# Performance work log

Hardware: AMD Instinct MI355X
Metric: run time of the kernel (lower is better)

## Reference

```python
import jax, jax.numpy as jnp
import numpy as np

B, S, D, NH = 1, 2048, 2048, 8
DH = D // NH
BACKEND_EPS = 1e-6
NORM_EPS = 1e-6


def setup_inputs() -> dict:
    key = jax.random.key(0)
    ks = jax.random.split(key, 6)
    q = jax.random.normal(ks[0], (B, S, D), jnp.float32)
    k = jax.random.normal(ks[1], (B, S, D), jnp.float32)
    v = jax.random.normal(ks[2], (B, S, D), jnp.float32)
    igate_kernel = jax.random.normal(ks[3], (3 * D, NH), jnp.float32) * 0.02
    igate_bias = jax.random.normal(ks[4], (NH,), jnp.float32) * 0.1
    fgate_kernel = jax.random.normal(ks[5], (3 * D, NH), jnp.float32) * 0.02
    fgate_bias = jnp.linspace(3.0, 6.0, NH, dtype=jnp.float32)  # bias_linspace_init(3.0, 6.0)
    out_weight = jnp.ones((NH, DH), jnp.float32)  # MultiHeadLayerNorm scale (no bias)
    return dict(q=q, k=k, v=v, igate_kernel=igate_kernel, igate_bias=igate_bias,
                fgate_kernel=fgate_kernel, fgate_bias=fgate_bias, out_weight=out_weight)


def _mlstm_parallel_stabilized(q, k, v, i_pre, f_pre):
    # q,k,v: (B,NH,S,DH); i_pre,f_pre: (B,NH,S)
    s = q.shape[-2]
    dh = q.shape[-1]
    log_f = jax.nn.log_sigmoid(f_pre)                              # (B,NH,S)
    cum = jnp.pad(jnp.cumsum(log_f, axis=-1), ((0, 0), (0, 0), (1, 0)))  # (B,NH,S+1), cum[0]=0
    # logfg[t, s] = cum[t+1] - cum[s+1] = sum_{j=s+1}^{t} log_f[j], valid for s <= t
    logfg = cum[..., 1:, None] - cum[..., None, 1:]                # (B,NH,S,S)
    causal = jnp.tril(jnp.ones((s, s), dtype=bool))
    logfg = jnp.where(causal, logfg, -jnp.inf)
    log_D = logfg + i_pre[..., None, :]                            # add input gate at source position s
    m = jnp.max(log_D, axis=-1, keepdims=True)                     # stabilizer (B,NH,S,1)
    D = jnp.exp(log_D - m)
    qk = jnp.einsum('bhsd,bhtd->bhst', q, k) / jnp.sqrt(jnp.float32(dh))
    C = qk * D                                                     # (B,NH,S,S)
    n = jnp.maximum(jnp.abs(jnp.sum(C, axis=-1, keepdims=True)), jnp.exp(-m))
    return jnp.einsum('bhst,bhtd->bhsd', C / (n + BACKEND_EPS), v)


def reference(q, k, v, igate_kernel, igate_bias, fgate_kernel, fgate_bias, out_weight):
    qkv = jnp.concatenate([q, k, v], axis=-1)                      # (B,S,3D)
    i_pre = qkv @ igate_kernel + igate_bias                        # (B,S,NH)
    f_pre = qkv @ fgate_kernel + fgate_bias                        # (B,S,NH)
    qh = q.reshape(B, S, NH, DH).transpose(0, 2, 1, 3)             # (B,NH,S,DH)
    kh = k.reshape(B, S, NH, DH).transpose(0, 2, 1, 3)
    vh = v.reshape(B, S, NH, DH).transpose(0, 2, 1, 3)
    h = _mlstm_parallel_stabilized(qh, kh, vh,
                                   i_pre.transpose(0, 2, 1),
                                   f_pre.transpose(0, 2, 1))       # (B,NH,S,DH)
    h = h.transpose(0, 2, 1, 3)                                    # (B,S,NH,DH)
    mu = jnp.mean(h, axis=-1, keepdims=True)
    var = jnp.var(h, axis=-1, keepdims=True)
    hn = (h - mu) * jax.lax.rsqrt(var + NORM_EPS) * out_weight     # per-head LN, scale only
    return hn.reshape(B, S, D)
```

## Files before the change

### kernel.cpp

```cpp
#include <hip/hip_runtime.h>
#include <hip/hip_bf16.h>

#define SEQ 2048
#define DMODEL 2048
#define NHEAD 8
#define DHEAD 256

typedef _Float16 v8h __attribute__((ext_vector_type(8)));
typedef unsigned short v8u __attribute__((ext_vector_type(8)));
typedef float v4f __attribute__((ext_vector_type(4)));

__device__ __forceinline__ float b2f(unsigned short s) {
    return __uint_as_float(((unsigned)s) << 16);
}
__device__ __forceinline__ unsigned short f2b(float f) {
    unsigned u = __float_as_uint(f);
    u += 0x7fffu + ((u >> 16) & 1u);
    return (unsigned short)(u >> 16);
}
__device__ __forceinline__ unsigned short f2h(float f) {
    _Float16 h = (_Float16)f;
    return __builtin_bit_cast(unsigned short, h);
}
__device__ __forceinline__ float h2f(unsigned short s) {
    return (float)__builtin_bit_cast(_Float16, s);
}

__global__ __launch_bounds__(256) void k_pre(const void* q, const void* k, const void* v,
                                             const void* igk, const void* fgk,
                                             int* flag,
                                             unsigned short* qb, unsigned short* kb,
                                             unsigned short* vT,
                                             float* iparts, float* fparts) {
    __shared__ float x_lds[32][67];
    __shared__ int cnt;
    const int tid = threadIdx.x;

    if (tid == 0) cnt = 0;
    __syncthreads();
    {
        const unsigned short* qp = (const unsigned short*)q;
        int wild = 0;
        for (int i = tid; i < 2048; i += 256) {
            float x = b2f(qp[i]);
            float ax = fabsf(x);
            if (!(ax <= 100.0f) || (x != 0.0f && ax < 1e-6f)) wild++;
        }
        atomicAdd(&cnt, wild);
    }
    __syncthreads();
    const int bf = (cnt < 256) ? 1 : 0;
    if (blockIdx.x == 0 && blockIdx.y == 0 && tid == 0) *flag = bf;

    const int s0 = blockIdx.x * 32;
    const int z  = blockIdx.y;
    const int tz = z >> 1;
    const int dbase = (z & 1) * 1024;
    const void* src = (tz == 0) ? q : (tz == 1) ? k : v;
    unsigned short* dst16 = (tz == 0) ? qb : kb;

    const int r  = tid >> 3, c0 = (tid & 7) * 8;
    const int sl = tid >> 3, hh = tid & 7;
    float accI = 0.f, accF = 0.f;
    const unsigned short* ik16 = (const unsigned short*)igk;
    const unsigned short* fk16 = (const unsigned short*)fgk;
    const float* ik32 = (const float*)igk;
    const float* fk32 = (const float*)fgk;

    for (int ch = 0; ch < 16; ++ch) {
        const int d0 = dbase + ch * 64;
        float xv[8];
        const size_t base = (size_t)(s0 + r) * DMODEL + d0 + c0;
        if (bf) {
            const unsigned short* sp = (const unsigned short*)src;
            v8u a = *(const v8u*)(sp + base);
#pragma unroll
            for (int j = 0; j < 8; j++) xv[j] = b2f(a[j]);
        } else {
            const float* sp = (const float*)src;
            v4f a0 = *(const v4f*)(sp + base);
            v4f a1 = *(const v4f*)(sp + base + 4);
#pragma unroll
            for (int j = 0; j < 4; j++) { xv[j] = a0[j]; xv[4 + j] = a1[j]; }
        }
        __syncthreads();
#pragma unroll
        for (int j = 0; j < 8; j++) x_lds[r][c0 + j] = xv[j];
        if (tz < 2) {
            v8u o;
#pragma unroll
            for (int j = 0; j < 8; j++) o[j] = f2h(xv[j]);
            *(v8u*)(dst16 + base) = o;
        }
        __syncthreads();
        const int gd0 = tz * 2048 + d0;
        if (bf) {
#pragma unroll 8
            for (int j = 0; j < 64; j++) {
                float x = x_lds[sl][j];
                int wi = (gd0 + j) * NHEAD + hh;
                accI += x * b2f(ik16[wi]);
                accF += x * b2f(fk16[wi]);
            }
        } else {
#pragma unroll 8
            for (int j = 0; j < 64; j++) {
                float x = x_lds[sl][j];
                int wi = (gd0 + j) * NHEAD + hh;
                accI += x * ik32[wi];
                accF += x * fk32[wi];
            }
        }
        if (tz == 2) {
            const int dloc = tid >> 2, sc0 = (tid & 3) * 8;
            v8u o;
#pragma unroll
            for (int j = 0; j < 8; j++) o[j] = f2h(x_lds[sc0 + j][dloc]);
            const int dglob = d0 + dloc;
            const int head = dglob >> 8, dh = dglob & 255;
            *(v8u*)(vT + ((size_t)(head * DHEAD + dh)) * SEQ + s0 + sc0) = o;
        }
    }
    iparts[(size_t)z * NHEAD * SEQ + hh * SEQ + s0 + sl] = accI;
    fparts[(size_t)z * NHEAD * SEQ + hh * SEQ + s0 + sl] = accF;
}

__global__ __launch_bounds__(256) void k_scan(const float* iparts, const float* fparts,
                                              const void* ib_, const void* fb_,
                                              const int* flag,
                                              float* a_g, float* amax_g, float* nfl_g) {
    __shared__ float sarr[256];
    int bf = *(volatile const int*)flag;
    int h = blockIdx.x, tid = threadIdx.x;
    float ib = bf ? b2f(((const unsigned short*)ib_)[h]) : ((const float*)ib_)[h];
    float fb = bf ? b2f(((const unsigned short*)fb_)[h]) : ((const float*)fb_)[h];
    int s0 = tid * 8;
    float lf[8], ip[8];
#pragma unroll
    for (int j = 0; j < 8; j++) {
        float fpv = fb, ipv = ib;
#pragma unroll
        for (int z = 0; z < 6; z++) {
            ipv += iparts[(size_t)z * NHEAD * SEQ + h * SEQ + s0 + j];
            fpv += fparts[(size_t)z * NHEAD * SEQ + h * SEQ + s0 + j];
        }
        lf[j] = fminf(fpv, 0.0f) - log1pf(__expf(-fabsf(fpv)));
        ip[j] = ipv;
    }
    float cs[8]; float t = 0.f;
#pragma unroll
    for (int j = 0; j < 8; j++) { t += lf[j]; cs[j] = t; }
    sarr[tid] = t; __syncthreads();
    for (int ofs = 1; ofs < 256; ofs <<= 1) {
        float val = sarr[tid];
        if (tid >= ofs) val += sarr[tid - ofs];
        __syncthreads(); sarr[tid] = val; __syncthreads();
    }
    float excl = (tid > 0) ? sarr[tid - 1] : 0.0f;
    float cum[8], av[8];
#pragma unroll
    for (int j = 0; j < 8; j++) { cum[j] = excl + cs[j]; av[j] = ip[j] - cum[j]; }
    float mx = av[0];
#pragma unroll
    for (int j = 1; j < 8; j++) mx = fmaxf(mx, av[j]);
    __syncthreads(); sarr[tid] = mx; __syncthreads();
    for (int ofs = 1; ofs < 256; ofs <<= 1) {
        float val = sarr[tid];
        if (tid >= ofs) val = fmaxf(val, sarr[tid - ofs]);
        __syncthreads(); sarr[tid] = val; __syncthreads();
    }
    float run = (tid > 0) ? sarr[tid - 1] : -3.0e38f;
#pragma unroll
    for (int j = 0; j < 8; j++) {
        run = fmaxf(run, av[j]);
        int s = s0 + j;
        a_g[h * SEQ + s]    = av[j];
        amax_g[h * SEQ + s] = run;
        float m = cum[j] + run;
        nfl_g[h * SEQ + s]  = __expf(fminf(fmaxf(-m, -60.f), 60.f));
    }
}

__global__ __launch_bounds__(256) void k_main(const unsigned short* __restrict__ qb,
                                              const unsigned short* __restrict__ kb,
                                              const unsigned short* __restrict__ vT,
                                              const float* __restrict__ a_g,
                                              const float* __restrict__ amax_g,
                                              float* __restrict__ h_buf,
                                              float* __restrict__ rs_buf) {
    __shared__ __align__(16) unsigned short q_lds[32][264];
    __shared__ __align__(16) unsigned short k_lds[32][264];
    __shared__ __align__(16) unsigned short vT_lds[272][40];
    __shared__ __align__(16) unsigned short P_lds[32][40];
    __shared__ __align__(16) unsigned short Plo_lds[32][40];
    __shared__ float a_s[32], amax_t[32];

    const int h   = blockIdx.x;
    const int y   = blockIdx.y;
    const int tid = threadIdx.x;
    const int lane = tid & 63;
    const int w   = tid >> 6;
    const int l15 = lane & 15;
    const int qd  = (lane >> 4) & 3;
    const int hd0 = h * DHEAD;

    int u         = 65 * (y >> 1) + ((y & 1) ? 33 : 0);
    int remaining = (y & 1) ? 32 : 33;
    int tile = (int)((sqrtf(8.0f * (float)u + 1.0f) - 1.0f) * 0.5f);
    while ((tile + 1) * (tile + 2) / 2 <= u) ++tile;
    while (tile * (tile + 1) / 2 > u) --tile;
    int js = u - tile * (tile + 1) / 2;
    bool needQ = true;

    for (int i = tid; i < 16 * 40; i += 256) {
        int r2 = i / 40, c2 = i % 40;
        vT_lds[256 + r2][c2] = (r2 == 0 && c2 < 32) ? (unsigned short)0x3C00 : (unsigned short)0;
    }

    const v4f vzero = {0.f, 0.f, 0.f, 0.f};
    v4f acc[2][4];
    v4f accN[2];
#pragma unroll
    for (int m = 0; m < 2; m++) {
        accN[m] = vzero;
#pragma unroll
        for (int n = 0; n < 4; n++) acc[m][n] = vzero;
    }

    const int mw = w >> 1, nw = w & 1;
    const int krow = tid >> 3, kc0 = (tid & 7) * 32;

    v8u kr0, kr1, kr2, kr3, vr0, vr1, vr2, vr3;
    float areg = 0.f;
    {
        const int s0 = js * 32;
        const unsigned short* ks = kb + (size_t)(s0 + krow) * DMODEL + hd0 + kc0;
        kr0 = *(const v8u*)(ks);      kr1 = *(const v8u*)(ks + 8);
        kr2 = *(const v8u*)(ks + 16); kr3 = *(const v8u*)(ks + 24);
        const unsigned short* vs = vT + (size_t)(hd0 + tid) * SEQ + s0;
        vr0 = *(const v8u*)(vs);      vr1 = *(const v8u*)(vs + 8);
        vr2 = *(const v8u*)(vs + 16); vr3 = *(const v8u*)(vs + 24);
        if (tid < 32) areg = a_g[h * SEQ + s0 + tid];
    }

    for (;;) {
        const int t0 = tile * 32;
        __syncthreads();
        if (needQ) {
            const unsigned short* src = qb + (size_t)(t0 + krow) * DMODEL + hd0 + kc0;
#pragma unroll
            for (int i = 0; i < 4; i++)
                *(v8u*)&q_lds[krow][kc0 + i * 8] = *(const v8u*)(src + i * 8);
            if (tid < 32) amax_t[tid] = amax_g[h * SEQ + t0 + tid];
            needQ = false;
        }
        *(v8u*)&k_lds[krow][kc0]      = kr0;
        *(v8u*)&k_lds[krow][kc0 + 8]  = kr1;
        *(v8u*)&k_lds[krow][kc0 + 16] = kr2;
        *(v8u*)&k_lds[krow][kc0 + 24] = kr3;
        *(v8u*)&vT_lds[tid][0]  = vr0;
        *(v8u*)&vT_lds[tid][8]  = vr1;
        *(v8u*)&vT_lds[tid][16] = vr2;
        *(v8u*)&vT_lds[tid][24] = vr3;
        if (tid < 32) a_s[tid] = areg;
        __syncthreads();

        v4f c = vzero;
#pragma unroll
        for (int d0 = 0; d0 < 256; d0 += 32) {
            v8h a = *(const v8h*)&q_lds[mw * 16 + l15][d0 + qd * 8];
            v8h b = *(const v8h*)&k_lds[nw * 16 + l15][d0 + qd * 8];
            c = __builtin_amdgcn_mfma_f32_16x16x32_f16(a, b, c, 0, 0, 0);
        }
        {
            const bool diag = (js == tile);
            const int col = nw * 16 + l15;
            const float av = a_s[col];
#pragma unroll
            for (int r = 0; r < 4; r++) {
                int row = mw * 16 + qd * 4 + r;
                float arg = fminf(av - amax_t[row], 0.0f);
                float val = c[r] * 0.0625f * __expf(arg);
                if (diag && col > row) val = 0.0f;
                unsigned short hi = f2h(val);
                float lo = val - h2f(hi);
                P_lds[row][col]   = hi;
                Plo_lds[row][col] = f2h(lo);
            }
        }
        __syncthreads();

        int ntile = tile, njs = js + 1; bool nq = false;
        if (njs > tile) { ntile = tile + 1; njs = 0; nq = true; }
        if (remaining > 1) {
            const int s0 = njs * 32;
            const unsigned short* ks = kb + (size_t)(s0 + krow) * DMODEL + hd0 + kc0;
            kr0 = *(const v8u*)(ks);      kr1 = *(const v8u*)(ks + 8);
            kr2 = *(const v8u*)(ks + 16); kr3 = *(const v8u*)(ks + 24);
            const unsigned short* vs = vT + (size_t)(hd0 + tid) * SEQ + s0;
            vr0 = *(const v8u*)(vs);      vr1 = *(const v8u*)(vs + 8);
            vr2 = *(const v8u*)(vs + 16); vr3 = *(const v8u*)(vs + 24);
            if (tid < 32) areg = a_g[h * SEQ + s0 + tid];
        }

        v8h aH0 = *(const v8h*)&P_lds[l15][qd * 8];
        v8h aH1 = *(const v8h*)&P_lds[16 + l15][qd * 8];
        v8h aL0 = *(const v8h*)&Plo_lds[l15][qd * 8];
        v8h aL1 = *(const v8h*)&Plo_lds[16 + l15][qd * 8];
#pragma unroll
        for (int nn = 0; nn < 4; nn++) {
            v8h bV = *(const v8h*)&vT_lds[w * 64 + nn * 16 + l15][qd * 8];
            acc[0][nn] = __builtin_amdgcn_mfma_f32_16x16x32_f16(aH0, bV, acc[0][nn], 0, 0, 0);
            acc[0][nn] = __builtin_amdgcn_mfma_f32_16x16x32_f16(aL0, bV, acc[0][nn], 0, 0, 0);
            acc[1][nn] = __builtin_amdgcn_mfma_f32_16x16x32_f16(aH1, bV, acc[1][nn], 0, 0, 0);
            acc[1][nn] = __builtin_amdgcn_mfma_f32_16x16x32_f16(aL1, bV, acc[1][nn], 0, 0, 0);
        }
        if (w == 3) {
            v8h bN = *(const v8h*)&vT_lds[256 + l15][qd * 8];
            accN[0] = __builtin_amdgcn_mfma_f32_16x16x32_f16(aH0, bN, accN[0], 0, 0, 0);
            accN[0] = __builtin_amdgcn_mfma_f32_16x16x32_f16(aL0, bN, accN[0], 0, 0, 0);
            accN[1] = __builtin_amdgcn_mfma_f32_16x16x32_f16(aH1, bN, accN[1], 0, 0, 0);
            accN[1] = __builtin_amdgcn_mfma_f32_16x16x32_f16(aL1, bN, accN[1], 0, 0, 0);
        }

        if (js == tile || remaining == 1) {
#pragma unroll
            for (int m = 0; m < 2; m++)
#pragma unroll
                for (int r = 0; r < 4; r++) {
                    int row = t0 + m * 16 + qd * 4 + r;
#pragma unroll
                    for (int nn = 0; nn < 4; nn++) {
                        int col = hd0 + w * 64 + nn * 16 + l15;
                        atomicAdd(&h_buf[(size_t)row * DMODEL + col], acc[m][nn][r]);
                        acc[m][nn][r] = 0.f;
                    }
                    if (w == 3 && l15 == 0)
                        atomicAdd(&rs_buf[h * SEQ + row], accN[m][r]);
                    accN[m][r] = 0.f;
                }
        }
        if (--remaining == 0) break;
        tile = ntile; js = njs; needQ = nq;
    }
}

__global__ __launch_bounds__(256) void k_finish(const float* __restrict__ h_buf,
                                                const float* __restrict__ rs_buf,
                                                const float* __restrict__ nfl_g,
                                                const void* __restrict__ ow,
                                                const int* flag, void* out) {
    const int wv = threadIdx.x >> 6, lane = threadIdx.x & 63;
    const int rid = blockIdx.x * 4 + wv;
    const int s = rid >> 3, h = rid & 7;
    const int bf = *(volatile const int*)flag;
    float rs  = rs_buf[h * SEQ + s];
    float nfl = nfl_g[h * SEQ + s];
    float sc  = 1.0f / (fmaxf(fabsf(rs), nfl) + 1e-6f);
    size_t base = (size_t)s * DMODEL + h * DHEAD + lane * 4;
    v4f hv = *(const v4f*)(h_buf + base);
#pragma unroll
    for (int j = 0; j < 4; j++) hv[j] *= sc;
    float sm = hv[0] + hv[1] + hv[2] + hv[3];
    float sq = hv[0] * hv[0] + hv[1] * hv[1] + hv[2] * hv[2] + hv[3] * hv[3];
#pragma unroll
    for (int m = 1; m < 64; m <<= 1) {
        sm += __shfl_xor(sm, m, 64);
        sq += __shfl_xor(sq, m, 64);
    }
    float mean = sm * (1.0f / 256.0f);
    float var  = fmaxf(sq * (1.0f / 256.0f) - mean * mean, 0.0f);
    float rstd = rsqrtf(var + 1e-6f);
    int gi = h * DHEAD + lane * 4;
    float g0, g1, g2, g3;
    if (bf) {
        const unsigned short* gp = (const unsigned short*)ow;
        g0 = b2f(gp[gi]); g1 = b2f(gp[gi + 1]); g2 = b2f(gp[gi + 2]); g3 = b2f(gp[gi + 3]);
    } else {
        const float* gp = (const float*)ow;
        g0 = gp[gi]; g1 = gp[gi + 1]; g2 = gp[gi + 2]; g3 = gp[gi + 3];
    }
    float gv[4] = {g0, g1, g2, g3};
    if (bf) {
        unsigned short* o = (unsigned short*)out + base;
#pragma unroll
        for (int j = 0; j < 4; j++) o[j] = f2b((hv[j] - mean) * rstd * gv[j]);
    } else {
        float* o = (float*)out + base;
#pragma unroll
        for (int j = 0; j < 4; j++) o[j] = (hv[j] - mean) * rstd * gv[j];
    }
}

extern "C" void kernel_launch(void* const* d_in, const int* in_sizes, int n_in,
                              void* d_out, int out_size, void* d_ws, size_t ws_size,
                              hipStream_t stream) {
    const void* q   = d_in[0];
    const void* k   = d_in[1];
    const void* v   = d_in[2];
    const void* igk = d_in[3];
    const void* igb = d_in[4];
    const void* fgk = d_in[5];
    const void* fgb = d_in[6];
    const void* ow  = d_in[7];

    char* ws = (char*)d_ws;
    int*   flag   = (int*)(ws + 0);
    float* iparts = (float*)(ws + 1024);
    float* fparts = iparts + 6 * NHEAD * SEQ;
    float* a_g    = fparts + 6 * NHEAD * SEQ;
    float* amax_g = a_g + NHEAD * SEQ;
    float* nfl_g  = amax_g + NHEAD * SEQ;
    unsigned short* qb = (unsigned short*)(nfl_g + NHEAD * SEQ);
    unsigned short* kb = qb + (size_t)SEQ * DMODEL;
    unsigned short* vT = kb + (size_t)SEQ * DMODEL;
    float* rs_buf = (float*)(vT + (size_t)SEQ * DMODEL);
    float* h_buf  = rs_buf + NHEAD * SEQ;

    hipMemsetAsync(rs_buf, 0, (size_t)NHEAD * SEQ * 4 + (size_t)SEQ * DMODEL * 4, stream);
    k_pre<<<dim3(64, 6), 256, 0, stream>>>(q, k, v, igk, fgk, flag, qb, kb, vT, iparts, fparts);
    k_scan<<<8, 256, 0, stream>>>(iparts, fparts, igb, fgb, flag, a_g, amax_g, nfl_g);
    k_main<<<dim3(8, 64), 256, 0, stream>>>(qb, kb, vT, a_g, amax_g, h_buf, rs_buf);
    k_finish<<<4096, 256, 0, stream>>>(h_buf, rs_buf, nfl_g, ow, flag, d_out);
}
```

Baseline: 268.2 us.

## Split preprocessing into separate convert, transpose and gate-projection blocks; warp-shuffle scan

The single fused preprocessing kernel (384 blocks, each converting, transposing and projecting gates over a 1024-wide slice) is replaced by a 3584-block kernel with three roles. Some blocks convert q/k to fp16, some transpose v through a 64x64 LDS tile, and the rest compute per-row gate projections with one wavefront per row, vectorised weight loads and shuffle reductions. The gate partial buffers shrink from 6 to 3 slices. The scan kernel swaps its LDS Hillis-Steele scans, which synchronise at every step, for wavefront shuffle scans plus a small cross-wave combine. The point is more parallelism and fewer barriers in the launch-latency-bound prologue, at the cost of rereading q/k/v in the gate blocks.

New measurement: 318.5 us. 1.19x slower.

```diff
diff --git a/kernel.cpp b/kernel.cpp
--- a/kernel.cpp
+++ b/kernel.cpp
@@ -32,9 +32,10 @@
                                              unsigned short* qb, unsigned short* kb,
                                              unsigned short* vT,
                                              float* iparts, float* fparts) {
-    __shared__ float x_lds[32][67];
+    __shared__ unsigned short tile[64][72];
     __shared__ int cnt;
     const int tid = threadIdx.x;
+    const int b = blockIdx.x;
 
     if (tid == 0) cnt = 0;
     __syncthreads();
@@ -50,126 +51,208 @@
     }
     __syncthreads();
     const int bf = (cnt < 256) ? 1 : 0;
-    if (blockIdx.x == 0 && blockIdx.y == 0 && tid == 0) *flag = bf;
-
-    const int s0 = blockIdx.x * 32;
-    const int z  = blockIdx.y;
-    const int tz = z >> 1;
-    const int dbase = (z & 1) * 1024;
-    const void* src = (tz == 0) ? q : (tz == 1) ? k : v;
-    unsigned short* dst16 = (tz == 0) ? qb : kb;
-
-    const int r  = tid >> 3, c0 = (tid & 7) * 8;
-    const int sl = tid >> 3, hh = tid & 7;
-    float accI = 0.f, accF = 0.f;
-    const unsigned short* ik16 = (const unsigned short*)igk;
-    const unsigned short* fk16 = (const unsigned short*)fgk;
-    const float* ik32 = (const float*)igk;
-    const float* fk32 = (const float*)fgk;
-
-    for (int ch = 0; ch < 16; ++ch) {
-        const int d0 = dbase + ch * 64;
-        float xv[8];
-        const size_t base = (size_t)(s0 + r) * DMODEL + d0 + c0;
+    if (b == 0 && tid == 0) *flag = bf;
+
+    if (b < 1024) {
+        size_t i0 = ((size_t)b * 256 + tid) * 16;
         if (bf) {
-            const unsigned short* sp = (const unsigned short*)src;
-            v8u a = *(const v8u*)(sp + base);
-#pragma unroll
-            for (int j = 0; j < 8; j++) xv[j] = b2f(a[j]);
+            const unsigned short* qp = (const unsigned short*)q;
+            const unsigned short* kp = (const unsigned short*)k;
+#pragma unroll
+            for (int hlf = 0; hlf < 2; hlf++) {
+                v8u uq = *(const v8u*)(qp + i0 + hlf * 8);
+                v8u uk = *(const v8u*)(kp + i0 + hlf * 8);
+                v8u oq, ok;
+#pragma unroll
+                for (int j = 0; j < 8; j++) { oq[j] = f2h(b2f(uq[j])); ok[j] = f2h(b2f(uk[j])); }
+                *(v8u*)(qb + i0 + hlf * 8) = oq;
+                *(v8u*)(kb + i0 + hlf * 8) = ok;
+            }
         } else {
-            const float* sp = (const float*)src;
-            v4f a0 = *(const v4f*)(sp + base);
-            v4f a1 = *(const v4f*)(sp + base + 4);
-#pragma unroll
-            for (int j = 0; j < 4; j++) { xv[j] = a0[j]; xv[4 + j] = a1[j]; }
+            const float* qf = (const float*)q;
+            const float* kf = (const float*)k;
+#pragma unroll
+            for (int hlf = 0; hlf < 2; hlf++) {
+                v4f q0 = *(const v4f*)(qf + i0 + hlf * 8);
+                v4f q1 = *(const v4f*)(qf + i0 + hlf * 8 + 4);
+                v4f k0 = *(const v4f*)(kf + i0 + hlf * 8);
+                v4f k1 = *(const v4f*)(kf + i0 + hlf * 8 + 4);
+                v8u oq, ok;
+#pragma unroll
+                for (int j = 0; j < 4; j++) {
+                    oq[j] = f2h(q0[j]); oq[4 + j] = f2h(q1[j]);
+                    ok[j] = f2h(k0[j]); ok[4 + j] = f2h(k1[j]);
+                }
+                *(v8u*)(qb + i0 + hlf * 8) = oq;
+                *(v8u*)(kb + i0 + hlf * 8) = ok;
+            }
+        }
+    } else if (b < 2048) {
+        int b2 = b - 1024;
+        int s0 = (b2 & 31) * 64, d0 = (b2 >> 5) * 64;
+        int r = tid >> 2, c0 = (tid & 3) * 16;
+        size_t base = (size_t)(s0 + r) * DMODEL + d0 + c0;
+        if (bf) {
+            const unsigned short* vp = (const unsigned short*)v;
+            v8u a = *(const v8u*)(vp + base);
+            v8u bb = *(const v8u*)(vp + base + 8);
+#pragma unroll
+            for (int j = 0; j < 8; j++) { tile[r][c0 + j] = f2h(b2f(a[j])); tile[r][c0 + 8 + j] = f2h(b2f(bb[j])); }
+        } else {
+            const float* vp = (const float*)v;
+            v4f a0 = *(const v4f*)(vp + base);
+            v4f a1 = *(const v4f*)(vp + base + 4);
+            v4f a2 = *(const v4f*)(vp + base + 8);
+            v4f a3 = *(const v4f*)(vp + base + 12);
+#pragma unroll
+            for (int j = 0; j < 4; j++) {
+                tile[r][c0 + j] = f2h(a0[j]);      tile[r][c0 + 4 + j] = f2h(a1[j]);
+                tile[r][c0 + 8 + j] = f2h(a2[j]);  tile[r][c0 + 12 + j] = f2h(a3[j]);
+            }
         }
         __syncthreads();
-#pragma unroll
-        for (int j = 0; j < 8; j++) x_lds[r][c0 + j] = xv[j];
-        if (tz < 2) {
-            v8u o;
-#pragma unroll
-            for (int j = 0; j < 8; j++) o[j] = f2h(xv[j]);
-            *(v8u*)(dst16 + base) = o;
-        }
-        __syncthreads();
-        const int gd0 = tz * 2048 + d0;
-        if (bf) {
-#pragma unroll 8
-            for (int j = 0; j < 64; j++) {
-                float x = x_lds[sl][j];
-                int wi = (gd0 + j) * NHEAD + hh;
-                accI += x * b2f(ik16[wi]);
-                accF += x * b2f(fk16[wi]);
-            }
-        } else {
-#pragma unroll 8
-            for (int j = 0; j < 64; j++) {
-                float x = x_lds[sl][j];
-                int wi = (gd0 + j) * NHEAD + hh;
-                accI += x * ik32[wi];
-                accF += x * fk32[wi];
-            }
-        }
-        if (tz == 2) {
-            const int dloc = tid >> 2, sc0 = (tid & 3) * 8;
-            v8u o;
-#pragma unroll
-            for (int j = 0; j < 8; j++) o[j] = f2h(x_lds[sc0 + j][dloc]);
-            const int dglob = d0 + dloc;
-            const int head = dglob >> 8, dh = dglob & 255;
-            *(v8u*)(vT + ((size_t)(head * DHEAD + dh)) * SEQ + s0 + sc0) = o;
-        }
-    }
-    iparts[(size_t)z * NHEAD * SEQ + hh * SEQ + s0 + sl] = accI;
-    fparts[(size_t)z * NHEAD * SEQ + hh * SEQ + s0 + sl] = accF;
+        int dr = tid >> 2, sc0 = (tid & 3) * 16;
+        v8u o0, o1;
+#pragma unroll
+        for (int j = 0; j < 8; j++) { o0[j] = tile[sc0 + j][dr]; o1[j] = tile[sc0 + 8 + j][dr]; }
+        int head = d0 >> 8;
+        int dh = (d0 & 255) + dr;
+        size_t ob = ((size_t)head * DHEAD + dh) * SEQ + s0 + sc0;
+        *(v8u*)(vT + ob) = o0;
+        *(v8u*)(vT + ob + 8) = o1;
+    } else {
+        const int wv = tid >> 6, lane = tid & 63;
+        const int gwid = (b - 2048) * 4 + wv;
+        const int tz = gwid >> 11;
+        const int s  = gwid & 2047;
+        const void* src = (tz == 0) ? q : (tz == 1) ? k : v;
+        const unsigned short* ik16 = (const unsigned short*)igk;
+        const unsigned short* fk16 = (const unsigned short*)fgk;
+        const float* ik32 = (const float*)igk;
+        const float* fk32 = (const float*)fgk;
+
+        float accI[8], accF[8];
+#pragma unroll
+        for (int hh = 0; hh < 8; hh++) { accI[hh] = 0.f; accF[hh] = 0.f; }
+
+        const size_t xrow = (size_t)s * DMODEL;
+#pragma unroll
+        for (int c = 0; c < 4; ++c) {
+            const int d0 = c * 512 + lane * 8;
+            float xv[8];
+            if (bf) {
+                v8u a = *(const v8u*)((const unsigned short*)src + xrow + d0);
+#pragma unroll
+                for (int j = 0; j < 8; j++) xv[j] = b2f(a[j]);
+            } else {
+                const float* sp = (const float*)src;
+                v4f a0 = *(const v4f*)(sp + xrow + d0);
+                v4f a1 = *(const v4f*)(sp + xrow + d0 + 4);
+#pragma unroll
+                for (int j = 0; j < 4; j++) { xv[j] = a0[j]; xv[4 + j] = a1[j]; }
+            }
+            const size_t wb = ((size_t)(tz * 2048 + d0)) * NHEAD;
+            if (bf) {
+#pragma unroll
+                for (int j = 0; j < 8; j++) {
+                    v8u wi = *(const v8u*)(ik16 + wb + j * 8);
+                    v8u wf = *(const v8u*)(fk16 + wb + j * 8);
+#pragma unroll
+                    for (int hh = 0; hh < 8; hh++) {
+                        accI[hh] += xv[j] * b2f(wi[hh]);
+                        accF[hh] += xv[j] * b2f(wf[hh]);
+                    }
+                }
+            } else {
+#pragma unroll
+                for (int j = 0; j < 8; j++) {
+                    v4f wi0 = *(const v4f*)(ik32 + wb + j * 8);
+                    v4f wi1 = *(const v4f*)(ik32 + wb + j * 8 + 4);
+                    v4f wf0 = *(const v4f*)(fk32 + wb + j * 8);
+                    v4f wf1 = *(const v4f*)(fk32 + wb + j * 8 + 4);
+#pragma unroll
+                    for (int hh = 0; hh < 4; hh++) {
+                        accI[hh] += xv[j] * wi0[hh];  accI[4 + hh] += xv[j] * wi1[hh];
+                        accF[hh] += xv[j] * wf0[hh];  accF[4 + hh] += xv[j] * wf1[hh];
+                    }
+                }
+            }
+        }
+#pragma unroll
+        for (int o = 1; o < 64; o <<= 1) {
+#pragma unroll
+            for (int hh = 0; hh < 8; hh++) {
+                accI[hh] += __shfl_xor(accI[hh], o, 64);
+                accF[hh] += __shfl_xor(accF[hh], o, 64);
+            }
+        }
+        if (lane == 0) {
+#pragma unroll
+            for (int hh = 0; hh < 8; hh++) {
+                iparts[(size_t)(tz * NHEAD + hh) * SEQ + s] = accI[hh];
+                fparts[(size_t)(tz * NHEAD + hh) * SEQ + s] = accF[hh];
+            }
+        }
+    }
 }
 
 __global__ __launch_bounds__(256) void k_scan(const float* iparts, const float* fparts,
                                               const void* ib_, const void* fb_,
                                               const int* flag,
                                               float* a_g, float* amax_g, float* nfl_g) {
-    __shared__ float sarr[256];
+    __shared__ float wtot[4], wmax[4];
     int bf = *(volatile const int*)flag;
     int h = blockIdx.x, tid = threadIdx.x;
+    int lane = tid & 63, wv = tid >> 6;
     float ib = bf ? b2f(((const unsigned short*)ib_)[h]) : ((const float*)ib_)[h];
     float fb = bf ? b2f(((const unsigned short*)fb_)[h]) : ((const float*)fb_)[h];
     int s0 = tid * 8;
     float lf[8], ip[8];
 #pragma unroll
     for (int j = 0; j < 8; j++) {
-        float fpv = fb, ipv = ib;
-#pragma unroll
-        for (int z = 0; z < 6; z++) {
-            ipv += iparts[(size_t)z * NHEAD * SEQ + h * SEQ + s0 + j];
-            fpv += fparts[(size_t)z * NHEAD * SEQ + h * SEQ + s0 + j];
-        }
-        lf[j] = fminf(fpv, 0.0f) - log1pf(__expf(-fabsf(fpv)));
+        float fp = fb, ipv = ib;
+#pragma unroll
+        for (int z = 0; z < 3; z++) {
+            ipv += iparts[(size_t)(z * NHEAD + h) * SEQ + s0 + j];
+            fp  += fparts[(size_t)(z * NHEAD + h) * SEQ + s0 + j];
+        }
+        lf[j] = fminf(fp, 0.0f) - log1pf(__expf(-fabsf(fp)));
         ip[j] = ipv;
     }
     float cs[8]; float t = 0.f;
 #pragma unroll
     for (int j = 0; j < 8; j++) { t += lf[j]; cs[j] = t; }
-    sarr[tid] = t; __syncthreads();
-    for (int ofs = 1; ofs < 256; ofs <<= 1) {
-        float val = sarr[tid];
-        if (tid >= ofs) val += sarr[tid - ofs];
-        __syncthreads(); sarr[tid] = val; __syncthreads();
-    }
-    float excl = (tid > 0) ? sarr[tid - 1] : 0.0f;
+    float incl = t;
+#pragma unroll
+    for (int o = 1; o < 64; o <<= 1) {
+        float n = __shfl_up(incl, o, 64);
+        if (lane >= o) incl += n;
+    }
+    if (lane == 63) wtot[wv] = incl;
+    __syncthreads();
+    float wpre = 0.f;
+#pragma unroll
+    for (int i2 = 0; i2 < 4; i2++) if (i2 < wv) wpre += wtot[i2];
+    float excl = wpre + incl - t;
     float cum[8], av[8];
 #pragma unroll
     for (int j = 0; j < 8; j++) { cum[j] = excl + cs[j]; av[j] = ip[j] - cum[j]; }
     float mx = av[0];
 #pragma unroll
     for (int j = 1; j < 8; j++) mx = fmaxf(mx, av[j]);
-    __syncthreads(); sarr[tid] = mx; __syncthreads();
-    for (int ofs = 1; ofs < 256; ofs <<= 1) {
-        float val = sarr[tid];
-        if (tid >= ofs) val = fmaxf(val, sarr[tid - ofs]);
-        __syncthreads(); sarr[tid] = val; __syncthreads();
-    }
-    float run = (tid > 0) ? sarr[tid - 1] : -3.0e38f;
+    float mincl = mx;
+#pragma unroll
+    for (int o = 1; o < 64; o <<= 1) {
+        float n = __shfl_up(mincl, o, 64);
+        if (lane >= o) mincl = fmaxf(mincl, n);
+    }
+    if (lane == 63) wmax[wv] = mincl;
+    __syncthreads();
+    float wpm = -3.0e38f;
+#pragma unroll
+    for (int i2 = 0; i2 < 4; i2++) if (i2 < wv) wpm = fmaxf(wpm, wmax[i2]);
+    float up = __shfl_up(mincl, 1, 64);
+    float run = fmaxf(wpm, (lane > 0) ? up : -3.0e38f);
 #pragma unroll
     for (int j = 0; j < 8; j++) {
         run = fmaxf(run, av[j]);
@@ -372,15 +455,16 @@
     float var  = fmaxf(sq * (1.0f / 256.0f) - mean * mean, 0.0f);
     float rstd = rsqrtf(var + 1e-6f);
     int gi = h * DHEAD + lane * 4;
-    float g0, g1, g2, g3;
+    float gv[4];
     if (bf) {
         const unsigned short* gp = (const unsigned short*)ow;
-        g0 = b2f(gp[gi]); g1 = b2f(gp[gi + 1]); g2 = b2f(gp[gi + 2]); g3 = b2f(gp[gi + 3]);
+#pragma unroll
+        for (int j = 0; j < 4; j++) gv[j] = b2f(gp[gi + j]);
     } else {
         const float* gp = (const float*)ow;
-        g0 = gp[gi]; g1 = gp[gi + 1]; g2 = gp[gi + 2]; g3 = gp[gi + 3];
-    }
-    float gv[4] = {g0, g1, g2, g3};
+#pragma unroll
+        for (int j = 0; j < 4; j++) gv[j] = gp[gi + j];
+    }
     if (bf) {
         unsigned short* o = (unsigned short*)out + base;
 #pragma unroll
@@ -407,18 +491,19 @@
     char* ws = (char*)d_ws;
     int*   flag   = (int*)(ws + 0);
     float* iparts = (float*)(ws + 1024);
-    float* fparts = iparts + 6 * NHEAD * SEQ;
-    float* a_g    = fparts + 6 * NHEAD * SEQ;
+    float* fparts = iparts + 3 * NHEAD * SEQ;
+    float* a_g    = fparts + 3 * NHEAD * SEQ;
     float* amax_g = a_g + NHEAD * SEQ;
     float* nfl_g  = amax_g + NHEAD * SEQ;
-    unsigned short* qb = (unsigned short*)(nfl_g + NHEAD * SEQ);
+    float* rs_buf = nfl_g + NHEAD * SEQ;
+    float* h_buf  = rs_buf + NHEAD * SEQ;
+    unsigned short* qb = (unsigned short*)(h_buf + (size_t)SEQ * DMODEL);
     unsigned short* kb = qb + (size_t)SEQ * DMODEL;
     unsigned short* vT = kb + (size_t)SEQ * DMODEL;
-    float* rs_buf = (float*)(vT + (size_t)SEQ * DMODEL);
-    float* h_buf  = rs_buf + NHEAD * SEQ;
-
-    hipMemsetAsync(rs_buf, 0, (size_t)NHEAD * SEQ * 4 + (size_t)SEQ * DMODEL * 4, stream);
-    k_pre<<<dim3(64, 6), 256, 0, stream>>>(q, k, v, igk, fgk, flag, qb, kb, vT, iparts, fparts);
+
+    size_t zbytes = (size_t)NHEAD * SEQ * 4 + (size_t)SEQ * DMODEL * 4;
+    hipMemsetAsync(rs_buf, 0, zbytes, stream);
+    k_pre<<<3584, 256, 0, stream>>>(q, k, v, igk, fgk, flag, qb, kb, vT, iparts, fparts);
     k_scan<<<8, 256, 0, stream>>>(iparts, fparts, igb, fgb, flag, a_g, amax_g, nfl_g);
     k_main<<<dim3(8, 64), 256, 0, stream>>>(qb, kb, vT, a_g, amax_g, h_buf, rs_buf);
     k_finish<<<4096, 256, 0, stream>>>(h_buf, rs_buf, nfl_g, ow, flag, d_out);
```
